# Kernel tuning notes

Measured on AMD Instinct MI355X. Metric: run time of the kernel, lower is better.

The kernel has to match this reference:

```python
import jax, jax.numpy as jnp
import numpy as np

N = 50000
HID = 128
NH = 4
E_RES, E_SEQ, E_KNN = 100000, 100000, 200000
BN_EPS = 1e-5
NEG_SLOPE = 0.2


def _gat(h, src, dst, W, al, ar, resW, b):
    """DGL-style GATConv (eval mode: feat_drop off, residual=True, bias).
    h: (N, in), W/resW: (in, H*out), al/ar: (H, out), b: (H*out,)"""
    Hh, out = al.shape
    feat = (h @ W).reshape(N, Hh, out)                 # (N, H, out)
    el = jnp.sum(feat * al, axis=-1)                   # (N, H)
    er = jnp.sum(feat * ar, axis=-1)                   # (N, H)
    e = jax.nn.leaky_relu(el[src] + er[dst], NEG_SLOPE)  # (E, H)
    # edge softmax over incoming edges of each dst node (numerically stable)
    m = jax.ops.segment_max(e, dst, num_segments=N)    # (N, H)
    ex = jnp.exp(e - m[dst])
    s = jax.ops.segment_sum(ex, dst, num_segments=N)
    a = ex / s[dst]                                    # (E, H)
    msg = a[:, :, None] * feat[src]                    # (E, H, out)
    rst = jax.ops.segment_sum(msg, dst, num_segments=N)  # (N, H, out)
    return rst + (h @ resW).reshape(N, Hh, out) + b.reshape(1, Hh, out)


def _hetero(h, src_res, dst_res, src_seq, dst_seq, src_knn, dst_knn, W, al, ar, resW, b):
    # HeteroGraphConv with aggregate='sum' over relations, then mean over heads
    r = _gat(h, src_res, dst_res, W[0], al[0], ar[0], resW[0], b[0])
    r = r + _gat(h, src_seq, dst_seq, W[1], al[1], ar[1], resW[1], b[1])
    r = r + _gat(h, src_knn, dst_knn, W[2], al[2], ar[2], resW[2], b[2])
    return jnp.mean(r, axis=1)                         # (N, out)


def setup_inputs() -> dict:
    key = jax.random.key(0)
    ks = iter(jax.random.split(key, 32))
    inp = {}
    inp["x"] = jax.random.normal(next(ks), (N, HID), jnp.float32)
    inp["src_res"] = jax.random.randint(next(ks), (E_RES,), 0, N, jnp.int32)
    inp["dst_res"] = jax.random.randint(next(ks), (E_RES,), 0, N, jnp.int32)
    inp["src_seq"] = jax.random.randint(next(ks), (E_SEQ,), 0, N, jnp.int32)
    inp["dst_seq"] = jax.random.randint(next(ks), (E_SEQ,), 0, N, jnp.int32)
    inp["src_knn"] = jax.random.randint(next(ks), (E_KNN,), 0, N, jnp.int32)
    inp["dst_knn"] = jax.random.randint(next(ks), (E_KNN,), 0, N, jnp.int32)
    sc = 0.05
    for l in (0, 1):
        inp[f"W{l}"] = jax.random.normal(next(ks), (3, HID, NH * HID), jnp.float32) * sc
        inp[f"al{l}"] = jax.random.normal(next(ks), (3, NH, HID), jnp.float32) * sc
        inp[f"ar{l}"] = jax.random.normal(next(ks), (3, NH, HID), jnp.float32) * sc
        inp[f"resW{l}"] = jax.random.normal(next(ks), (3, HID, NH * HID), jnp.float32) * sc
        inp[f"b{l}"] = jax.random.normal(next(ks), (3, NH * HID), jnp.float32) * sc
    inp["fc_W"] = jax.random.normal(next(ks), (HID, HID), jnp.float32) * sc
    inp["fc_b"] = jax.random.normal(next(ks), (HID,), jnp.float32) * sc
    inp["bn_gamma"] = jnp.ones((HID,), jnp.float32)
    inp["bn_beta"] = jnp.zeros((HID,), jnp.float32)
    inp["bn_mean"] = jax.random.normal(next(ks), (HID,), jnp.float32) * sc
    inp["bn_var"] = jax.random.uniform(next(ks), (HID,), jnp.float32)
    return inp


def reference(x, src_res, dst_res, src_seq, dst_seq, src_knn, dst_knn,
              W0, al0, ar0, resW0, b0, W1, al1, ar1, resW1, b1,
              fc_W, fc_b, bn_gamma, bn_beta, bn_mean, bn_var):
    # layer 0: hetero GAT, head-mean, fc + ReLU + BatchNorm (eval), dropout=identity
    h = _hetero(x, src_res, dst_res, src_seq, dst_seq, src_knn, dst_knn,
                W0, al0, ar0, resW0, b0)
    h = jax.nn.relu(h @ fc_W + fc_b)
    h = (h - bn_mean) / jnp.sqrt(bn_var + BN_EPS) * bn_gamma + bn_beta
    # layer 1 (final): hetero GAT, head-mean
    out = _hetero(h, src_res, dst_res, src_seq, dst_seq, src_knn, dst_knn,
                  W1, al1, ar1, resW1, b1)
    return out
```

## Files before the change

kernel.cpp:

```cpp
#include <hip/hip_runtime.h>
#include <hip/hip_bf16.h>
#include <math.h>
#include <stdint.h>

#define NNODES 50000
#define SCHUNK 4096
#define AW 1664
#define XOFF 1536

typedef __bf16 bf16x8 __attribute__((ext_vector_type(8)));
typedef float f32x4 __attribute__((ext_vector_type(4)));
typedef unsigned short u16;
typedef unsigned int u32;

__device__ __forceinline__ float lrelu(float x){ return x >= 0.f ? x : 0.2f*x; }
__device__ __forceinline__ float lo2f(u32 v){ union{ u32 i; float f; } c; c.i = v<<16; return c.f; }
__device__ __forceinline__ float hi2f(u32 v){ union{ u32 i; float f; } c; c.i = v & 0xffff0000u; return c.f; }
__device__ __forceinline__ u16 f2b(float f){ __hip_bfloat16 h = __float2bfloat16(f); return *(u16*)&h; }
__device__ __forceinline__ u32 packbf(float a, float b){ return (u32)f2b(a) | ((u32)f2b(b) << 16); }

#define GLDS16(g, l) __builtin_amdgcn_global_load_lds( \
    (const __attribute__((address_space(1))) void*)(g), \
    (__attribute__((address_space(3))) void*)(l), 16, 0, 0)

__global__ void prep_all(const float* __restrict__ W0, const float* __restrict__ W1,
                         const float* __restrict__ resW0, const float* __restrict__ resW1,
                         const float* __restrict__ b0, const float* __restrict__ b1,
                         const float* __restrict__ al0, const float* __restrict__ ar0,
                         const float* __restrict__ al1, const float* __restrict__ ar1,
                         const float* __restrict__ fcW,
                         u16* __restrict__ Btb, float* __restrict__ biasf,
                         u16* __restrict__ wlb, u16* __restrict__ fcWtb,
                         int* __restrict__ cnt)
{
    int gid = blockIdx.x*blockDim.x + threadIdx.x;
    if (gid < 3*NNODES) cnt[gid] = 0;
    if (gid < 2*128*AW){
        int l = gid / (128*AW);
        int rem = gid - l*(128*AW);
        int c = rem / AW;
        int j = rem - c*AW;
        const float* W  = l ? W1 : W0;
        const float* rw = l ? resW1 : resW0;
        float v;
        if (j < XOFF){
            int r = j >> 9, h = (j >> 7) & 3, k = j & 127;
            v = 0.25f * W[(size_t)r*65536 + (size_t)k*512 + h*128 + c];
        } else {
            int k = j - XOFF;
            float s = 0.f;
            for (int r = 0; r < 3; ++r)
                for (int h = 0; h < 4; ++h)
                    s += rw[(size_t)r*65536 + (size_t)k*512 + h*128 + c];
            v = 0.25f * s;
        }
        Btb[gid] = f2b(v);
    }
    if (gid < 256){
        int l = gid >> 7, c = gid & 127;
        const float* bb = l ? b1 : b0;
        float s = 0.f;
        for (int r = 0; r < 3; ++r)
            for (int h = 0; h < 4; ++h)
                s += bb[r*512 + h*128 + c];
        biasf[gid] = 0.25f*s;
    }
    if (gid < 2*128*128){
        int l = gid >> 14;
        int col = (gid >> 7) & 127;
        int k = gid & 127;
        float v = 0.f;
        if (col < 24){
            int r = col >> 3, lr = (col >> 2) & 1, h = col & 3;
            const float* W = l ? W1 : W0;
            const float* av = l ? (lr ? ar1 : al1) : (lr ? ar0 : al0);
            const float* wrow = W + (size_t)r*65536 + (size_t)k*512 + h*128;
            const float* arow = av + r*512 + h*128;
            for (int cc = 0; cc < 128; ++cc) v += wrow[cc]*arow[cc];
        }
        wlb[gid] = f2b(v);
    }
    if (gid < 128*128){
        int k = gid & 127, n = gid >> 7;
        fcWtb[gid] = f2b(fcW[k*128 + n]);
    }
}

__global__ __launch_bounds__(256) void xprep_kernel(const float* __restrict__ x,
    u16* __restrict__ Ax, const u16* __restrict__ wl, float* __restrict__ el, int M)
{
    __shared__ u16 Xs[64*136];
    __shared__ u16 Ws[32*136];
    const int tid = threadIdx.x;
    const int row0 = blockIdx.x*64;
    #pragma unroll
    for (int p = 0; p < 2; ++p){
        int idx = tid + p*256;
        int c = idx >> 4, kc = (idx & 15)*8;
        float4 v = make_float4(0.f,0.f,0.f,0.f);
        if (c < 24) v = *(const float4*)(wl + c*128 + kc);
        *(float4*)&Ws[c*136 + kc] = v;
    }
    int r = tid >> 2, cq = (tid & 3)*32;
    int grow = row0 + r;
    if (grow < M){
        #pragma unroll
        for (int i = 0; i < 8; ++i){
            float4 v = *(const float4*)(x + (size_t)grow*128 + cq + i*4);
            ushort4 o;
            o.x = f2b(v.x); o.y = f2b(v.y); o.z = f2b(v.z); o.w = f2b(v.w);
            *(ushort4*)(Ax + (size_t)grow*AW + cq + i*4) = o;
            *(ushort4*)&Xs[r*136 + cq + i*4] = o;
        }
    } else {
        ushort4 z; z.x=0; z.y=0; z.z=0; z.w=0;
        #pragma unroll
        for (int i = 0; i < 8; ++i) *(ushort4*)&Xs[r*136 + cq + i*4] = z;
    }
    __syncthreads();
    const int lane = tid & 63, wave = tid >> 6;
    const int r16 = lane & 15, quad = lane >> 4;
    f32x4 acc0 = {}, acc1 = {};
    #pragma unroll
    for (int ks = 0; ks < 4; ++ks){
        int ko = ks*32 + quad*8;
        bf16x8 a  = *(const bf16x8*)&Xs[(wave*16 + r16)*136 + ko];
        bf16x8 b0 = *(const bf16x8*)&Ws[r16*136 + ko];
        bf16x8 b1 = *(const bf16x8*)&Ws[(16 + r16)*136 + ko];
        acc0 = __builtin_amdgcn_mfma_f32_16x16x32_bf16(a, b0, acc0, 0,0,0);
        acc1 = __builtin_amdgcn_mfma_f32_16x16x32_bf16(a, b1, acc1, 0,0,0);
    }
    #pragma unroll
    for (int p = 0; p < 4; ++p){
        int row = row0 + wave*16 + quad*4 + p;
        if (row < M){
            el[(size_t)row*32 + r16] = acc0[p];
            if (r16 < 8) el[(size_t)row*32 + 16 + r16] = acc1[p];
        }
    }
}

__global__ void hist_all(const int* __restrict__ d0, const int* __restrict__ d1,
                         const int* __restrict__ d2, int e0, int e1, int e2,
                         int* __restrict__ cnt)
{
    int g = blockIdx.x*blockDim.x + threadIdx.x;
    if (g >= e0 + e1 + e2) return;
    int rel, idx;
    if (g < e0){ rel = 0; idx = g; }
    else if (g < e0 + e1){ rel = 1; idx = g - e0; }
    else { rel = 2; idx = g - e0 - e1; }
    const int* d = rel == 0 ? d0 : (rel == 1 ? d1 : d2);
    atomicAdd(cnt + (size_t)rel*NNODES + d[idx], 1);
}

__global__ __launch_bounds__(256) void scan_part(const int* __restrict__ cnt_all,
                                                 int* __restrict__ partials, int Nn, int nblk)
{
    int rel = blockIdx.y, blk = blockIdx.x;
    const int* cnt = cnt_all + (size_t)rel*Nn;
    int tid = threadIdx.x;
    int i0 = blk*SCHUNK + tid*16;
    int s = 0;
    #pragma unroll
    for (int k = 0; k < 4; ++k){
        int idx = i0 + k*4;
        if (idx + 3 < Nn){ int4 v = *(const int4*)(cnt + idx); s += v.x+v.y+v.z+v.w; }
        else { for (int j = 0; j < 4; ++j) if (idx+j < Nn) s += cnt[idx+j]; }
    }
    #pragma unroll
    for (int off = 1; off < 64; off <<= 1) s += __shfl_xor(s, off);
    __shared__ int ws[4];
    if ((tid & 63) == 0) ws[tid>>6] = s;
    __syncthreads();
    if (tid == 0) partials[rel*nblk + blk] = ws[0]+ws[1]+ws[2]+ws[3];
}

__global__ __launch_bounds__(256) void scan_write(const int* __restrict__ cnt_all,
                                                  const int* __restrict__ partials,
                                                  int* __restrict__ rp_all, int* __restrict__ cur_all,
                                                  int Nn, int nblk)
{
    int rel = blockIdx.y, blk = blockIdx.x;
    const int* cnt = cnt_all + (size_t)rel*Nn;
    int* rp  = rp_all  + (size_t)rel*(Nn+1);
    int* cur = cur_all + (size_t)rel*Nn;
    int tid = threadIdx.x;
    __shared__ int sOff;
    __shared__ int wsum[4];
    if (tid == 0){
        int o = 0;
        for (int b = 0; b < blk; ++b) o += partials[rel*nblk + b];
        sOff = o;
        if (blk == 0){
            int t = 0;
            for (int b = 0; b < nblk; ++b) t += partials[rel*nblk + b];
            rp[Nn] = t;
        }
    }
    int i0 = blk*SCHUNK + tid*16;
    int v[16];
    int s = 0;
    #pragma unroll
    for (int k = 0; k < 16; ++k){
        int idx = i0 + k;
        v[k] = (idx < Nn) ? cnt[idx] : 0;
        s += v[k];
    }
    int lane = tid & 63;
    int incl = s;
    #pragma unroll
    for (int off = 1; off < 64; off <<= 1){
        int t = __shfl_up(incl, off);
        if (lane >= off) incl += t;
    }
    if (lane == 63) wsum[tid>>6] = incl;
    __syncthreads();
    int woff = 0;
    for (int w = 0; w < (tid>>6); ++w) woff += wsum[w];
    int ex = sOff + woff + incl - s;
    #pragma unroll
    for (int k = 0; k < 16; ++k){
        int idx = i0 + k;
        if (idx < Nn){ rp[idx] = ex; cur[idx] = ex; }
        ex += v[k];
    }
}

__global__ void scatter_all(const int* __restrict__ s0, const int* __restrict__ s1,
                            const int* __restrict__ s2,
                            const int* __restrict__ d0, const int* __restrict__ d1,
                            const int* __restrict__ d2, int e0, int e1, int e2,
                            int* __restrict__ cur, int* __restrict__ colb,
                            int* __restrict__ dste)
{
    int g = blockIdx.x*blockDim.x + threadIdx.x;
    if (g >= e0 + e1 + e2) return;
    int rel, idx, coff;
    if (g < e0){ rel = 0; idx = g; coff = 0; }
    else if (g < e0 + e1){ rel = 1; idx = g - e0; coff = e0; }
    else { rel = 2; idx = g - e0 - e1; coff = e0 + e1; }
    const int* sp = rel == 0 ? s0 : (rel == 1 ? s1 : s2);
    const int* dp = rel == 0 ? d0 : (rel == 1 ? d1 : d2);
    int d = dp[idx];
    int pos = atomicAdd(cur + (size_t)rel*NNODES + d, 1);
    colb[coff + pos] = sp[idx];
    dste[coff + pos] = d;
}

__global__ void wprep(const int* __restrict__ colb, const int* __restrict__ dste,
                      int e0, int e01, int etot,
                      const float* __restrict__ el_all, uint4* __restrict__ rec)
{
    int j = blockIdx.x*blockDim.x + threadIdx.x;
    if (j >= etot) return;
    int rel = (j < e0) ? 0 : ((j < e01) ? 1 : 2);
    int src = colb[j], dst = dste[j];
    float4 es = *(const float4*)(el_all + (size_t)src*32 + rel*8);
    float4 ed = *(const float4*)(el_all + (size_t)dst*32 + rel*8 + 4);
    uint4 o;
    o.x = (u32)src;
    o.y = packbf(__expf(lrelu(es.x + ed.x)), __expf(lrelu(es.y + ed.y)));
    o.z = packbf(__expf(lrelu(es.z + ed.z)), __expf(lrelu(es.w + ed.w)));
    o.w = 0;
    rec[j] = o;
}

__global__ __launch_bounds__(256) void agg3(const int* __restrict__ rowp_all,
    const uint4* __restrict__ rec_all, int e0, int e01,
    const u16* __restrict__ Ax, u16* __restrict__ Abuf, int Nn)
{
    const int rel = blockIdx.y;
    const int tid = threadIdx.x;
    const int o = tid & 15;
    const int n = (blockIdx.x*256 + tid) >> 4;
    if (n >= Nn) return;
    const int* rowp = rowp_all + (size_t)rel*(Nn+1);
    const int coff = (rel == 0) ? 0 : ((rel == 1) ? e0 : e01);
    const uint4* rec = rec_all + coff;
    u16* op = Abuf + (size_t)n*AW + rel*512 + o*8;

    int beg = rowp[n], end = rowp[n+1];
    if (beg >= end){
        uint4 z; z.x = 0; z.y = 0; z.z = 0; z.w = 0;
        #pragma unroll
        for (int h = 0; h < 4; ++h) *(uint4*)(op + h*128) = z;
        return;
    }
    float acc[4][8] = {};
    float us0 = 0.f, us1 = 0.f, us2 = 0.f, us3 = 0.f;

    uint4 ra = rec[beg];
    uint4 xa = *(const uint4*)(Ax + (size_t)ra.x*AW + o*8);
    uint4 rb = ra, xb = xa;
    if (beg + 1 < end){
        rb = rec[beg+1];
        xb = *(const uint4*)(Ax + (size_t)rb.x*AW + o*8);
    }
    for (int j = beg; j < end; ++j){
        uint4 rc = rb, xc = xb;
        if (j + 2 < end){
            rc = rec[j+2];
            xc = *(const uint4*)(Ax + (size_t)rc.x*AW + o*8);
        }
        float w0 = lo2f(ra.y), w1 = hi2f(ra.y), w2 = lo2f(ra.z), w3 = hi2f(ra.z);
        us0 += w0; us1 += w1; us2 += w2; us3 += w3;
        float xv[8];
        xv[0] = lo2f(xa.x); xv[1] = hi2f(xa.x);
        xv[2] = lo2f(xa.y); xv[3] = hi2f(xa.y);
        xv[4] = lo2f(xa.z); xv[5] = hi2f(xa.z);
        xv[6] = lo2f(xa.w); xv[7] = hi2f(xa.w);
        #pragma unroll
        for (int c = 0; c < 8; ++c){
            acc[0][c] = fmaf(w0, xv[c], acc[0][c]);
            acc[1][c] = fmaf(w1, xv[c], acc[1][c]);
            acc[2][c] = fmaf(w2, xv[c], acc[2][c]);
            acc[3][c] = fmaf(w3, xv[c], acc[3][c]);
        }
        ra = rb; xa = xb; rb = rc; xb = xc;
    }
    float inv[4] = {1.f/us0, 1.f/us1, 1.f/us2, 1.f/us3};
    #pragma unroll
    for (int h = 0; h < 4; ++h){
        uint4 ov;
        ov.x = packbf(acc[h][0]*inv[h], acc[h][1]*inv[h]);
        ov.y = packbf(acc[h][2]*inv[h], acc[h][3]*inv[h]);
        ov.z = packbf(acc[h][4]*inv[h], acc[h][5]*inv[h]);
        ov.w = packbf(acc[h][6]*inv[h], acc[h][7]*inv[h]);
        *(uint4*)(op + h*128) = ov;
    }
}

template<int EPI, int FCF>
__global__ __launch_bounds__(256, 3) void gemm_f(
    const u16* __restrict__ A, int Astride, int K,
    const u16* __restrict__ Bt,
    float* __restrict__ Cf, u16* __restrict__ Cb, int Cstride, int M,
    const float* __restrict__ bias, const float* __restrict__ gamma,
    const float* __restrict__ beta, const float* __restrict__ mean,
    const float* __restrict__ var,
    const u16* __restrict__ wl, float* __restrict__ el,
    const u16* __restrict__ fcw, const float* __restrict__ fcb2)
{
    __shared__ u16 smem[FCF ? 26112 : 16384];
    const int tid = threadIdx.x;
    const int row0 = blockIdx.x*128;
    const int lane = tid & 63, wave = tid >> 6;
    const int wm = (wave >> 1)*64, wn = (wave & 1)*64;
    const int r16 = lane & 15, quad = lane >> 4;
    const int swzbase = r16 & 7;
    f32x4 acc[4][4] = {};

    const int r8 = lane >> 3, jc = lane & 7;
    const int soff = ((jc ^ r8) << 3);
    const u16* srcA[4];
    const u16* srcB[4];
    #pragma unroll
    for (int g = 0; g < 4; ++g){
        int gr = row0 + wave*32 + g*8 + r8;
        if (gr >= M) gr = M - 1;
        srcA[g] = A + (size_t)gr*Astride + soff;
        srcB[g] = Bt + (size_t)(wave*32 + g*8 + r8)*K + soff;
    }
    u16* As = smem;
    u16* Bs = smem + 8192;
    const int nk = K >> 6;

    for (int t = 0; t < nk; ++t){
        const int k0 = t << 6;
        #pragma unroll
        for (int g = 0; g < 4; ++g){
            GLDS16(srcA[g] + k0, As + wave*2048 + g*512);
            GLDS16(srcB[g] + k0, Bs + wave*2048 + g*512);
        }
        __syncthreads();
        #pragma unroll
        for (int ks = 0; ks < 2; ++ks){
            int swz = ((ks*4 + quad) ^ swzbase) << 3;
            bf16x8 a[4], b[4];
            #pragma unroll
            for (int i = 0; i < 4; ++i) a[i] = *(const bf16x8*)&As[(wm + i*16 + r16)*64 + swz];
            #pragma unroll
            for (int j = 0; j < 4; ++j) b[j] = *(const bf16x8*)&Bs[(wn + j*16 + r16)*64 + swz];
            #pragma unroll
            for (int i = 0; i < 4; ++i)
                #pragma unroll
                for (int j = 0; j < 4; ++j)
                    acc[i][j] = __builtin_amdgcn_mfma_f32_16x16x32_bf16(a[i], b[j], acc[i][j], 0,0,0);
        }
        __syncthreads();
    }

    if (!FCF){
        #pragma unroll
        for (int i = 0; i < 4; ++i){
            #pragma unroll
            for (int p = 0; p < 4; ++p){
                int row = row0 + wm + i*16 + quad*4 + p;
                #pragma unroll
                for (int j = 0; j < 4; ++j){
                    int col = wn + j*16 + r16;
                    float v = acc[i][j][p] + bias[col];
                    if (row < M){
                        if (EPI == 1) Cf[(size_t)row*Cstride + col] = v;
                        else          Cb[(size_t)row*Cstride + col] = f2b(v);
                    }
                }
            }
        }
    } else {
        u16* Cs = smem;
        u16* Ws = smem + 17408;
        #pragma unroll
        for (int i = 0; i < 4; ++i){
            #pragma unroll
            for (int p = 0; p < 4; ++p){
                int rl = wm + i*16 + quad*4 + p;
                #pragma unroll
                for (int j = 0; j < 4; ++j){
                    int col = wn + j*16 + r16;
                    Cs[rl*136 + col] = f2b(acc[i][j][p] + bias[col]);
                }
            }
        }
        __syncthreads();
        f32x4 fa[2][8] = {};
        #pragma unroll
        for (int hh = 0; hh < 2; ++hh){
            {
                int rr = tid >> 2, sg = (tid & 3)*32;
                const u16* src = fcw + (size_t)(hh*64 + rr)*128 + sg;
                #pragma unroll
                for (int q = 0; q < 4; ++q)
                    *(float4*)&Ws[rr*136 + sg + q*8] = *(const float4*)(src + q*8);
            }
            __syncthreads();
            #pragma unroll
            for (int ks = 0; ks < 4; ++ks){
                int ko = ks*32 + quad*8;
                #pragma unroll
                for (int i = 0; i < 2; ++i){
                    bf16x8 a = *(const bf16x8*)&Cs[(wave*32 + i*16 + r16)*136 + ko];
                    #pragma unroll
                    for (int jj = 0; jj < 4; ++jj){
                        bf16x8 b = *(const bf16x8*)&Ws[(jj*16 + r16)*136 + ko];
                        fa[i][hh*4+jj] = __builtin_amdgcn_mfma_f32_16x16x32_bf16(a, b, fa[i][hh*4+jj], 0,0,0);
                    }
                }
            }
            __syncthreads();
        }
        #pragma unroll
        for (int f = 0; f < 8; ++f){
            int col = f*16 + r16;
            float fb = fcb2[col];
            float mn = mean[col];
            float sc = gamma[col]*rsqrtf(var[col] + 1e-5f);
            float bt = beta[col];
            #pragma unroll
            for (int i = 0; i < 2; ++i){
                #pragma unroll
                for (int p = 0; p < 4; ++p){
                    int rl = wave*32 + i*16 + quad*4 + p;
                    int row = row0 + rl;
                    float v = fa[i][f][p] + fb;
                    v = fmaxf(v, 0.f);
                    v = (v - mn)*sc + bt;
                    u16 vb = f2b(v);
                    if (row < M) Cb[(size_t)row*Cstride + col] = vb;
                    Cs[rl*136 + col] = vb;
                }
            }
        }
        #pragma unroll
        for (int p = 0; p < 2; ++p){
            int idx = tid + p*256;
            int c = idx >> 4, kc = (idx & 15)*8;
            float4 v = make_float4(0.f,0.f,0.f,0.f);
            if (c < 24) v = *(const float4*)(wl + c*128 + kc);
            *(float4*)&Ws[c*136 + kc] = v;
        }
        __syncthreads();
        f32x4 e0[2] = {}, e1[2] = {};
        #pragma unroll
        for (int ks = 0; ks < 4; ++ks){
            int ko = ks*32 + quad*8;
            #pragma unroll
            for (int i = 0; i < 2; ++i){
                bf16x8 a  = *(const bf16x8*)&Cs[(wave*32 + i*16 + r16)*136 + ko];
                bf16x8 b0 = *(const bf16x8*)&Ws[r16*136 + ko];
                bf16x8 b1 = *(const bf16x8*)&Ws[(16 + r16)*136 + ko];
                e0[i] = __builtin_amdgcn_mfma_f32_16x16x32_bf16(a, b0, e0[i], 0,0,0);
                e1[i] = __builtin_amdgcn_mfma_f32_16x16x32_bf16(a, b1, e1[i], 0,0,0);
            }
        }
        #pragma unroll
        for (int i = 0; i < 2; ++i){
            #pragma unroll
            for (int p = 0; p < 4; ++p){
                int row = row0 + wave*32 + i*16 + quad*4 + p;
                if (row < M){
                    el[(size_t)row*32 + r16] = e0[i][p];
                    if (r16 < 8) el[(size_t)row*32 + 16 + r16] = e1[i][p];
                }
            }
        }
    }
}

static inline char* align256(char* p){ return (char*)(((uintptr_t)p + 255) & ~(uintptr_t)255); }

extern "C" void kernel_launch(void* const* d_in, const int* in_sizes, int n_in,
                              void* d_out, int out_size, void* d_ws, size_t ws_size,
                              hipStream_t stream)
{
    const float* x      = (const float*)d_in[0];
    const int* srcs[3]  = {(const int*)d_in[1], (const int*)d_in[3], (const int*)d_in[5]};
    const int* dsts[3]  = {(const int*)d_in[2], (const int*)d_in[4], (const int*)d_in[6]};
    const int  E[3]     = {in_sizes[1], in_sizes[3], in_sizes[5]};
    const float* W0     = (const float*)d_in[7];
    const float* al0    = (const float*)d_in[8];
    const float* ar0    = (const float*)d_in[9];
    const float* resW0  = (const float*)d_in[10];
    const float* b0     = (const float*)d_in[11];
    const float* W1     = (const float*)d_in[12];
    const float* al1    = (const float*)d_in[13];
    const float* ar1    = (const float*)d_in[14];
    const float* resW1  = (const float*)d_in[15];
    const float* b1     = (const float*)d_in[16];
    const float* fcW    = (const float*)d_in[17];
    const float* fcb    = (const float*)d_in[18];
    const float* gamma  = (const float*)d_in[19];
    const float* beta   = (const float*)d_in[20];
    const float* bmean  = (const float*)d_in[21];
    const float* bvar   = (const float*)d_in[22];
    float* out = (float*)d_out;

    char* p = (char*)d_ws;
    u16*   Abuf  = (u16*)p;   p += (size_t)NNODES*AW*2;    p = align256(p);
    float* el    = (float*)p; p += (size_t)NNODES*32*4;    p = align256(p);
    int*   cnt   = (int*)p;   p += (size_t)3*NNODES*4;     p = align256(p);
    int*   rowp  = (int*)p;   p += (size_t)3*(NNODES+1)*4; p = align256(p);
    int*   cur   = (int*)p;   p += (size_t)3*NNODES*4;     p = align256(p);
    int*   colb  = (int*)p;   p += (size_t)(E[0]+E[1]+E[2])*4; p = align256(p);
    int*   dste  = (int*)p;   p += (size_t)(E[0]+E[1]+E[2])*4; p = align256(p);
    uint4* rec   = (uint4*)p; p += (size_t)(E[0]+E[1]+E[2])*16; p = align256(p);
    u16*   Btb   = (u16*)p;   p += (size_t)2*128*AW*2;     p = align256(p);
    u16*   wlb   = (u16*)p;   p += (size_t)2*128*128*2;    p = align256(p);
    u16*   fcWtb = (u16*)p;   p += (size_t)128*128*2;      p = align256(p);
    float* biasf = (float*)p; p += (size_t)2*128*4;        p = align256(p);
    int*   parts = (int*)p;   p += (size_t)3*64*4;

    const int NBLK = (NNODES + SCHUNK - 1)/SCHUNK;
    const int MB64 = (NNODES + 63)/64;
    const int MBG  = (NNODES + 127)/128;
    const int AGGBLKS = (NNODES*16 + 255)/256;
    const int ETOT = E[0] + E[1] + E[2];
    dim3 blk(256);
    u16* Ax = Abuf + XOFF;

    prep_all<<<(2*128*AW + 255)/256, blk, 0, stream>>>(W0, W1, resW0, resW1, b0, b1,
                                                       al0, ar0, al1, ar1, fcW,
                                                       Btb, biasf, wlb, fcWtb, cnt);
    xprep_kernel<<<MB64, blk, 0, stream>>>(x, Ax, wlb, el, NNODES);
    hist_all<<<(ETOT + 255)/256, blk, 0, stream>>>(dsts[0], dsts[1], dsts[2], E[0], E[1], E[2], cnt);
    scan_part <<<dim3(NBLK,3), blk, 0, stream>>>(cnt, parts, NNODES, NBLK);
    scan_write<<<dim3(NBLK,3), blk, 0, stream>>>(cnt, parts, rowp, cur, NNODES, NBLK);
    scatter_all<<<(ETOT + 255)/256, blk, 0, stream>>>(srcs[0], srcs[1], srcs[2],
                                                      dsts[0], dsts[1], dsts[2],
                                                      E[0], E[1], E[2], cur, colb, dste);

    wprep<<<(ETOT + 255)/256, blk, 0, stream>>>(colb, dste, E[0], E[0]+E[1], ETOT, el, rec);
    agg3<<<dim3(AGGBLKS,3), blk, 0, stream>>>(rowp, rec, E[0], E[0]+E[1], Ax, Abuf, NNODES);
    gemm_f<0,1><<<MBG, blk, 0, stream>>>(Abuf, AW, AW, Btb, nullptr, Ax, AW, NNODES,
                                         biasf, gamma, beta, bmean, bvar,
                                         wlb + 16384, el, fcWtb, fcb);

    wprep<<<(ETOT + 255)/256, blk, 0, stream>>>(colb, dste, E[0], E[0]+E[1], ETOT, el, rec);
    agg3<<<dim3(AGGBLKS,3), blk, 0, stream>>>(rowp, rec, E[0], E[0]+E[1], Ax, Abuf, NNODES);
    gemm_f<1,0><<<MBG, blk, 0, stream>>>(Abuf, AW, AW, Btb + (size_t)128*AW, out, nullptr, 128, NNODES,
                                         biasf + 128, nullptr, nullptr, nullptr, nullptr,
                                         nullptr, nullptr, nullptr, nullptr);
}
```

Baseline: 361.3 us.

## Fuse edge weight computation into aggregation and double-buffer GEMM with register-resident B

Drops the wprep kernel and the dste/rec edge buffers. agg3 now reads source indices from colb and computes the exp(leaky_relu(el_src+er_dst)) attention weights inline from the el array. This removes a launch and the extra edge-record traffic per layer, at the cost of one extra gathered float4 load and four exps per edge per thread. Separately, the GEMM weight matrix is repacked into an MFMA-fragment-friendly layout so B tiles are loaded straight into registers, and A staging to LDS is double-buffered so the next tile's loads overlap the current MFMAs.

```diff
diff --git a/kernel.cpp b/kernel.cpp
--- a/kernel.cpp
+++ b/kernel.cpp
@@ -54,7 +54,7 @@
                     s += rw[(size_t)r*65536 + (size_t)k*512 + h*128 + c];
             v = 0.25f * s;
         }
-        Btb[gid] = f2b(v);
+        Btb[(size_t)l*128*AW + (size_t)(j>>3)*1024 + c*8 + (j&7)] = f2b(v);
     }
     if (gid < 256){
         int l = gid >> 7, c = gid & 127;
@@ -231,8 +231,7 @@
                             const int* __restrict__ s2,
                             const int* __restrict__ d0, const int* __restrict__ d1,
                             const int* __restrict__ d2, int e0, int e1, int e2,
-                            int* __restrict__ cur, int* __restrict__ colb,
-                            int* __restrict__ dste)
+                            int* __restrict__ cur, int* __restrict__ colb)
 {
     int g = blockIdx.x*blockDim.x + threadIdx.x;
     if (g >= e0 + e1 + e2) return;
@@ -245,29 +244,11 @@
     int d = dp[idx];
     int pos = atomicAdd(cur + (size_t)rel*NNODES + d, 1);
     colb[coff + pos] = sp[idx];
-    dste[coff + pos] = d;
-}
-
-__global__ void wprep(const int* __restrict__ colb, const int* __restrict__ dste,
-                      int e0, int e01, int etot,
-                      const float* __restrict__ el_all, uint4* __restrict__ rec)
-{
-    int j = blockIdx.x*blockDim.x + threadIdx.x;
-    if (j >= etot) return;
-    int rel = (j < e0) ? 0 : ((j < e01) ? 1 : 2);
-    int src = colb[j], dst = dste[j];
-    float4 es = *(const float4*)(el_all + (size_t)src*32 + rel*8);
-    float4 ed = *(const float4*)(el_all + (size_t)dst*32 + rel*8 + 4);
-    uint4 o;
-    o.x = (u32)src;
-    o.y = packbf(__expf(lrelu(es.x + ed.x)), __expf(lrelu(es.y + ed.y)));
-    o.z = packbf(__expf(lrelu(es.z + ed.z)), __expf(lrelu(es.w + ed.w)));
-    o.w = 0;
-    rec[j] = o;
 }
 
 __global__ __launch_bounds__(256) void agg3(const int* __restrict__ rowp_all,
-    const uint4* __restrict__ rec_all, int e0, int e01,
+    const int* __restrict__ colb_all, int e0, int e01,
+    const float* __restrict__ el_all,
     const u16* __restrict__ Ax, u16* __restrict__ Abuf, int Nn)
 {
     const int rel = blockIdx.y;
@@ -277,7 +258,7 @@
     if (n >= Nn) return;
     const int* rowp = rowp_all + (size_t)rel*(Nn+1);
     const int coff = (rel == 0) ? 0 : ((rel == 1) ? e0 : e01);
-    const uint4* rec = rec_all + coff;
+    const int* colb = colb_all + coff;
     u16* op = Abuf + (size_t)n*AW + rel*512 + o*8;
 
     int beg = rowp[n], end = rowp[n+1];
@@ -287,23 +268,30 @@
         for (int h = 0; h < 4; ++h) *(uint4*)(op + h*128) = z;
         return;
     }
+    float4 ed = *(const float4*)(el_all + (size_t)n*32 + rel*8 + 4);
     float acc[4][8] = {};
     float us0 = 0.f, us1 = 0.f, us2 = 0.f, us3 = 0.f;
 
-    uint4 ra = rec[beg];
-    uint4 xa = *(const uint4*)(Ax + (size_t)ra.x*AW + o*8);
-    uint4 rb = ra, xb = xa;
+    int sa = colb[beg];
+    uint4 xa = *(const uint4*)(Ax + (size_t)sa*AW + o*8);
+    float4 ea = *(const float4*)(el_all + (size_t)sa*32 + rel*8);
+    int sb = sa; uint4 xb = xa; float4 eb = ea;
     if (beg + 1 < end){
-        rb = rec[beg+1];
-        xb = *(const uint4*)(Ax + (size_t)rb.x*AW + o*8);
+        sb = colb[beg+1];
+        xb = *(const uint4*)(Ax + (size_t)sb*AW + o*8);
+        eb = *(const float4*)(el_all + (size_t)sb*32 + rel*8);
     }
     for (int j = beg; j < end; ++j){
-        uint4 rc = rb, xc = xb;
+        int sc = sb; uint4 xc = xb; float4 ec = eb;
         if (j + 2 < end){
-            rc = rec[j+2];
-            xc = *(const uint4*)(Ax + (size_t)rc.x*AW + o*8);
-        }
-        float w0 = lo2f(ra.y), w1 = hi2f(ra.y), w2 = lo2f(ra.z), w3 = hi2f(ra.z);
+            sc = colb[j+2];
+            xc = *(const uint4*)(Ax + (size_t)sc*AW + o*8);
+            ec = *(const float4*)(el_all + (size_t)sc*32 + rel*8);
+        }
+        float w0 = __expf(lrelu(ea.x + ed.x));
+        float w1 = __expf(lrelu(ea.y + ed.y));
+        float w2 = __expf(lrelu(ea.z + ed.z));
+        float w3 = __expf(lrelu(ea.w + ed.w));
         us0 += w0; us1 += w1; us2 += w2; us3 += w3;
         float xv[8];
         xv[0] = lo2f(xa.x); xv[1] = hi2f(xa.x);
@@ -317,7 +305,7 @@
             acc[2][c] = fmaf(w2, xv[c], acc[2][c]);
             acc[3][c] = fmaf(w3, xv[c], acc[3][c]);
         }
-        ra = rb; xa = xb; rb = rc; xb = xc;
+        xa = xb; ea = eb; sb = sc; xb = xc; eb = ec;
     }
     float inv[4] = {1.f/us0, 1.f/us1, 1.f/us2, 1.f/us3};
     #pragma unroll
@@ -354,42 +342,62 @@
     const int r8 = lane >> 3, jc = lane & 7;
     const int soff = ((jc ^ r8) << 3);
     const u16* srcA[4];
-    const u16* srcB[4];
     #pragma unroll
     for (int g = 0; g < 4; ++g){
         int gr = row0 + wave*32 + g*8 + r8;
         if (gr >= M) gr = M - 1;
         srcA[g] = A + (size_t)gr*Astride + soff;
-        srcB[g] = Bt + (size_t)(wave*32 + g*8 + r8)*K + soff;
-    }
-    u16* As = smem;
-    u16* Bs = smem + 8192;
+    }
+    const u16* bbase = Bt + (size_t)quad*1024 + (size_t)(wn + r16)*8;
     const int nk = K >> 6;
 
-    for (int t = 0; t < nk; ++t){
-        const int k0 = t << 6;
-        #pragma unroll
-        for (int g = 0; g < 4; ++g){
-            GLDS16(srcA[g] + k0, As + wave*2048 + g*512);
-            GLDS16(srcB[g] + k0, Bs + wave*2048 + g*512);
-        }
+    #define STAGEA(buf, t) do { \
+        u16* As_ = smem + (buf)*8192; \
+        const int k0_ = (t) << 6; \
+        _Pragma("unroll") \
+        for (int g_ = 0; g_ < 4; ++g_) GLDS16(srcA[g_] + k0_, As_ + wave*2048 + g_*512); \
+    } while (0)
+
+    #define LOADB(dst, t) do { \
+        _Pragma("unroll") \
+        for (int ks_ = 0; ks_ < 2; ++ks_) \
+            _Pragma("unroll") \
+            for (int j_ = 0; j_ < 4; ++j_) \
+                dst[ks_][j_] = *(const bf16x8*)(bbase + (size_t)(t)*8192 + ks_*4096 + j_*128); \
+    } while (0)
+
+    #define MFMA_STEP(bufv, B) do { \
+        const u16* As_ = smem + (bufv)*8192; \
+        _Pragma("unroll") \
+        for (int ks_ = 0; ks_ < 2; ++ks_){ \
+            int swz_ = ((ks_*4 + quad) ^ swzbase) << 3; \
+            bf16x8 a_[4]; \
+            _Pragma("unroll") \
+            for (int i_ = 0; i_ < 4; ++i_) a_[i_] = *(const bf16x8*)&As_[(wm + i_*16 + r16)*64 + swz_]; \
+            _Pragma("unroll") \
+            for (int i_ = 0; i_ < 4; ++i_) \
+                _Pragma("unroll") \
+                for (int j_ = 0; j_ < 4; ++j_) \
+                    acc[i_][j_] = __builtin_amdgcn_mfma_f32_16x16x32_bf16(a_[i_], B[ks_][j_], acc[i_][j_], 0,0,0); \
+        } \
+    } while (0)
+
+    bf16x8 b0r[2][4], b1r[2][4];
+    LOADB(b0r, 0);
+    STAGEA(0, 0);
+    __syncthreads();
+    for (int t = 0; t < nk; t += 2){
+        if (t + 1 < nk){ STAGEA(1, t+1); LOADB(b1r, t+1); }
+        MFMA_STEP(0, b0r);
         __syncthreads();
-        #pragma unroll
-        for (int ks = 0; ks < 2; ++ks){
-            int swz = ((ks*4 + quad) ^ swzbase) << 3;
-            bf16x8 a[4], b[4];
-            #pragma unroll
-            for (int i = 0; i < 4; ++i) a[i] = *(const bf16x8*)&As[(wm + i*16 + r16)*64 + swz];
-            #pragma unroll
-            for (int j = 0; j < 4; ++j) b[j] = *(const bf16x8*)&Bs[(wn + j*16 + r16)*64 + swz];
-            #pragma unroll
-            for (int i = 0; i < 4; ++i)
-                #pragma unroll
-                for (int j = 0; j < 4; ++j)
-                    acc[i][j] = __builtin_amdgcn_mfma_f32_16x16x32_bf16(a[i], b[j], acc[i][j], 0,0,0);
-        }
+        if (t + 1 >= nk) break;
+        if (t + 2 < nk){ STAGEA(0, t+2); LOADB(b0r, t+2); }
+        MFMA_STEP(1, b1r);
         __syncthreads();
     }
+    #undef STAGEA
+    #undef LOADB
+    #undef MFMA_STEP
 
     if (!FCF){
         #pragma unroll
@@ -543,8 +551,6 @@
     int*   rowp  = (int*)p;   p += (size_t)3*(NNODES+1)*4; p = align256(p);
     int*   cur   = (int*)p;   p += (size_t)3*NNODES*4;     p = align256(p);
     int*   colb  = (int*)p;   p += (size_t)(E[0]+E[1]+E[2])*4; p = align256(p);
-    int*   dste  = (int*)p;   p += (size_t)(E[0]+E[1]+E[2])*4; p = align256(p);
-    uint4* rec   = (uint4*)p; p += (size_t)(E[0]+E[1]+E[2])*16; p = align256(p);
     u16*   Btb   = (u16*)p;   p += (size_t)2*128*AW*2;     p = align256(p);
     u16*   wlb   = (u16*)p;   p += (size_t)2*128*128*2;    p = align256(p);
     u16*   fcWtb = (u16*)p;   p += (size_t)128*128*2;      p = align256(p);
@@ -568,16 +574,14 @@
     scan_write<<<dim3(NBLK,3), blk, 0, stream>>>(cnt, parts, rowp, cur, NNODES, NBLK);
     scatter_all<<<(ETOT + 255)/256, blk, 0, stream>>>(srcs[0], srcs[1], srcs[2],
                                                       dsts[0], dsts[1], dsts[2],
-                                                      E[0], E[1], E[2], cur, colb, dste);
-
-    wprep<<<(ETOT + 255)/256, blk, 0, stream>>>(colb, dste, E[0], E[0]+E[1], ETOT, el, rec);
-    agg3<<<dim3(AGGBLKS,3), blk, 0, stream>>>(rowp, rec, E[0], E[0]+E[1], Ax, Abuf, NNODES);
+                                                      E[0], E[1], E[2], cur, colb);
+
+    agg3<<<dim3(AGGBLKS,3), blk, 0, stream>>>(rowp, colb, E[0], E[0]+E[1], el, Ax, Abuf, NNODES);
     gemm_f<0,1><<<MBG, blk, 0, stream>>>(Abuf, AW, AW, Btb, nullptr, Ax, AW, NNODES,
                                          biasf, gamma, beta, bmean, bvar,
                                          wlb + 16384, el, fcWtb, fcb);
 
-    wprep<<<(ETOT + 255)/256, blk, 0, stream>>>(colb, dste, E[0], E[0]+E[1], ETOT, el, rec);
-    agg3<<<dim3(AGGBLKS,3), blk, 0, stream>>>(rowp, rec, E[0], E[0]+E[1], Ax, Abuf, NNODES);
+    agg3<<<dim3(AGGBLKS,3), blk, 0, stream>>>(rowp, colb, E[0], E[0]+E[1], el, Ax, Abuf, NNODES);
     gemm_f<1,0><<<MBG, blk, 0, stream>>>(Abuf, AW, AW, Btb + (size_t)128*AW, out, nullptr, 128, NNODES,
                                          biasf + 128, nullptr, nullptr, nullptr, nullptr,
                                          nullptr, nullptr, nullptr, nullptr);
```

Measured after the change: 742.3 us. 2.05x slower.
